# Optimization experiments

Hardware: AMD Instinct MI355X
Metric: run time of the kernel (lower is better)

## Reference

```python
import jax, jax.numpy as jnp
import numpy as np

B, N, F_DIM = 64, 4096, 64
K_SLOTS, D, N_ITERS = 8, 64, 3
EPS = 1e-8
LN_EPS = 1e-5  # torch LayerNorm default


def layernorm(x, g, b):
    mu = jnp.mean(x, axis=-1, keepdims=True)
    var = jnp.mean(jnp.square(x - mu), axis=-1, keepdims=True)
    return (x - mu) * jax.lax.rsqrt(var + LN_EPS) * g + b


def gru_cell(x, h, w_ih, w_hh, b_ih, b_hh):
    # torch.nn.GRUCell semantics; weights are [3D, D] with gate order r, z, n
    gi = x @ w_ih.T + b_ih
    gh = h @ w_hh.T + b_hh
    i_r, i_z, i_n = jnp.split(gi, 3, axis=-1)
    h_r, h_z, h_n = jnp.split(gh, 3, axis=-1)
    r = jax.nn.sigmoid(i_r + h_r)
    z = jax.nn.sigmoid(i_z + h_z)
    n = jnp.tanh(i_n + r * h_n)
    return (1.0 - z) * n + z * h


def setup_inputs() -> dict:
    key = jax.random.key(0)
    ks = jax.random.split(key, 16)
    f32 = jnp.float32
    s = 0.05  # small init scale for weights
    return {
        "inputs": jax.random.normal(ks[0], (B, N, F_DIM), f32),
        "slots_noise": jax.random.normal(ks[1], (B, K_SLOTS, D), f32),
        "slots_mu": jax.random.normal(ks[2], (1, 1, D), f32) * s,
        "slots_log_sigma": jax.random.normal(ks[3], (1, 1, D), f32) * s,
        "Wq": jax.random.normal(ks[4], (D, D), f32) * s,
        "Wk": jax.random.normal(ks[5], (D, F_DIM), f32) * s,
        "Wv": jax.random.normal(ks[6], (D, F_DIM), f32) * s,
        "gru_w_ih": jax.random.normal(ks[7], (3 * D, D), f32) * s,
        "gru_w_hh": jax.random.normal(ks[8], (3 * D, D), f32) * s,
        "gru_b_ih": jnp.zeros((3 * D,), f32),
        "gru_b_hh": jnp.zeros((3 * D,), f32),
        "mlp_w1": jax.random.normal(ks[9], (2 * D, D), f32) * s,
        "mlp_b1": jnp.zeros((2 * D,), f32),
        "mlp_w2": jax.random.normal(ks[10], (D, 2 * D), f32) * s,
        "mlp_b2": jnp.zeros((D,), f32),
        "ln_in_g": jnp.ones((F_DIM,), f32), "ln_in_b": jnp.zeros((F_DIM,), f32),
        "ln_slots_g": jnp.ones((D,), f32), "ln_slots_b": jnp.zeros((D,), f32),
        "ln_mlp_g": jnp.ones((D,), f32), "ln_mlp_b": jnp.zeros((D,), f32),
    }


def reference(inputs, slots_noise, slots_mu, slots_log_sigma, Wq, Wk, Wv,
              gru_w_ih, gru_w_hh, gru_b_ih, gru_b_hh,
              mlp_w1, mlp_b1, mlp_w2, mlp_b2,
              ln_in_g, ln_in_b, ln_slots_g, ln_slots_b, ln_mlp_g, ln_mlp_b):
    x = layernorm(inputs, ln_in_g, ln_in_b)          # [B, N, F]
    k = jnp.einsum('bnf,df->bnd', x, Wk)             # [B, N, D]
    v = jnp.einsum('bnf,df->bnd', x, Wv)             # [B, N, D]

    slots = slots_mu + jnp.exp(slots_log_sigma) * slots_noise  # [B, K, D]
    scale = D ** -0.5

    for _ in range(N_ITERS):
        slots_prev = slots
        s_n = layernorm(slots, ln_slots_g, ln_slots_b)
        q = jnp.einsum('bkd,ed->bke', s_n, Wq)                  # [B, K, D]
        attn_logits = jnp.einsum('bnd,bkd->bnk', k, q) * scale  # [B, N, K]
        attn = jax.nn.softmax(attn_logits, axis=-1) + EPS       # softmax over slots
        attn = attn / jnp.sum(attn, axis=1, keepdims=True)      # renormalize over N
        updates = jnp.einsum('bnk,bnd->bkd', attn, v)           # [B, K, D]
        slots = gru_cell(updates.reshape(-1, D), slots_prev.reshape(-1, D),
                         gru_w_ih, gru_w_hh, gru_b_ih, gru_b_hh).reshape(B, K_SLOTS, D)
        h = layernorm(slots, ln_mlp_g, ln_mlp_b)
        h = jax.nn.relu(h @ mlp_w1.T + mlp_b1) @ mlp_w2.T + mlp_b2
        slots = slots + h
    return slots
```

## Files before the change

### kernel.cpp

```cpp
#include <hip/hip_runtime.h>
#include <math.h>

#define NN 4096
#define LN_EPS 1e-5f
#define EPS 1e-8f

typedef unsigned short ushortT;
typedef unsigned int uintT;
typedef __attribute__((ext_vector_type(8))) short short8;
typedef __attribute__((ext_vector_type(4))) float f32x4;
typedef __attribute__((ext_vector_type(4))) unsigned short us4;

#define OFF_XN    0L
#define OFF_QU    8388608L
#define OFF_ACC   8421376L
#define OFF_COL   8519680L
#define OFF_SLOTS 8521216L
#define OFF_WIHT  8553984L
#define OFF_WHHT  8566272L
#define OFF_W1T   8578560L
#define OFF_W2T   8586752L
#define OFF_WQT   8594944L
#define OFF_WVT   8599040L
#define OFF_CNT   8603136L
#define OFF_RDY   8603328L

__device__ __forceinline__ float wredsum(float v) {
#pragma unroll
  for (int off = 32; off > 0; off >>= 1) v += __shfl_xor(v, off);
  return v;
}

__device__ __forceinline__ ushortT f2bf(float f) {
  uintT b = __float_as_uint(f);
  b += 0x7fff + ((b >> 16) & 1);
  return (ushortT)(b >> 16);
}

__device__ __forceinline__ uintT pack2bf(float lo, float hi) {
  return (uintT)f2bf(lo) | ((uintT)f2bf(hi) << 16);
}

__global__ __launch_bounds__(256) void k_prep(
    const float* __restrict__ w_ih, const float* __restrict__ w_hh,
    const float* __restrict__ w1, const float* __restrict__ w2,
    const float* __restrict__ Wq, const float* __restrict__ Wv,
    float* __restrict__ wihT, float* __restrict__ whhT,
    float* __restrict__ w1T, float* __restrict__ w2T, float* __restrict__ wqT,
    float* __restrict__ wvT, uintT* __restrict__ cnt, uintT* __restrict__ ready)
{
  int idx = blockIdx.x * 256 + threadIdx.x;
  if (idx < 12288) {
    int j = idx >> 6, f = idx & 63;
    wihT[f * 192 + j] = w_ih[idx];
  } else if (idx < 24576) {
    int i = idx - 12288; int j = i >> 6, f = i & 63;
    whhT[f * 192 + j] = w_hh[i];
  } else if (idx < 32768) {
    int i = idx - 24576; int j = i >> 6, f = i & 63;
    w1T[f * 128 + j] = w1[i];
  } else if (idx < 40960) {
    int i = idx - 32768; int d = i >> 7, j = i & 127;
    w2T[j * 64 + d] = w2[i];
  } else if (idx < 45056) {
    int i = idx - 40960; int e = i >> 6, d = i & 63;
    wqT[d * 64 + e] = Wq[i];
  } else if (idx < 49152) {
    int i = idx - 45056; int d = i >> 6, f = i & 63;
    wvT[f * 64 + d] = Wv[i];
  } else if (idx < 49344) {
    cnt[idx - 49152] = 0u;
  } else if (idx < 49408) {
    ready[idx - 49344] = 0u;
  }
}

__global__ __launch_bounds__(256) void k_ln_init(
    const float* __restrict__ inp,
    const float* __restrict__ g, const float* __restrict__ bbv,
    ushortT* __restrict__ xnG,
    const float* __restrict__ noise, const float* __restrict__ smu,
    const float* __restrict__ slsig, const float* __restrict__ wqT,
    const float* __restrict__ Wk,
    const float* __restrict__ g_sl, const float* __restrict__ b_sl,
    float* __restrict__ slots, uintT* __restrict__ qU,
    float* __restrict__ acc, float* __restrict__ colsum)
{
  __shared__ __align__(16) ushortT xnF[4096];
  const int tid = threadIdx.x;
  const int lane = tid & 63;
  const int wave = tid >> 6;

  if (blockIdx.x >= 4096) {
    const int bi = blockIdx.x - 4096;
    const int row = bi * 4 + wave;
    const int b = row >> 3, ks = row & 7;
    float* SI = (float*)&xnF[0];
    float* Sw = SI + (wave << 9);

    float s0 = fmaf(expf(slsig[lane]), noise[row * 64 + lane], smu[lane]);
    slots[row * 64 + lane] = s0;
#pragma unroll
    for (int it = 0; it < 3; ++it) {
      acc[it * 32768 + row * 64 + lane] = 0.f;
      if (lane == 0) colsum[it * 512 + row] = 0.f;
    }

    float mu = wredsum(s0) * (1.f / 64.f);
    float dx = s0 - mu;
    float var = wredsum(dx * dx) * (1.f / 64.f);
    float sn = dx * rsqrtf(var + LN_EPS) * g_sl[lane] + b_sl[lane];
    Sw[lane] = sn;
    float qe = 0.f;
#pragma unroll 16
    for (int d = 0; d < 64; ++d) qe = fmaf(Sw[d], wqT[d * 64 + lane], qe);
    Sw[64 + lane] = qe;
    float qp = 0.f;
#pragma unroll 16
    for (int e = 0; e < 64; ++e) qp = fmaf(Sw[64 + e], Wk[e * 64 + lane], qp);
    Sw[128 + lane] = qp * 0.125f;
    if (lane < 32) {
      const int kb = lane >> 4, lrow = (lane >> 2) & 3, j2 = lane & 3;
      const int fA = kb * 32 + lrow * 8 + 2 * j2;
      uintT u = pack2bf(Sw[128 + fA], Sw[128 + fA + 1]);
      qU[((b * 2 + kb) * 64 + lrow * 16 + ks) * 4 + j2] = u;
      qU[((b * 2 + kb) * 64 + lrow * 16 + 8 + ks) * 4 + j2] = 0u;
    }
    return;
  }

  const int l15 = lane & 15, q = lane >> 4;
  const int tile = blockIdx.x;
  const int b = tile >> 6;
  const int c = tile & 63;
  const int n0 = c << 6;
  const float* rowbase = inp + (((long)b * NN + n0) << 6);
  const float4 g4 = *(const float4*)&g[l15 << 2];
  const float4 b4 = *(const float4*)&bbv[l15 << 2];

#pragma unroll
  for (int i = 0; i < 4; ++i) {
    const int row = (wave << 4) + (i << 2) + q;
    float4 x = *(const float4*)&rowbase[(row << 6) + (l15 << 2)];
    float s = x.x + x.y + x.z + x.w;
    s += __shfl_xor(s, 1); s += __shfl_xor(s, 2);
    s += __shfl_xor(s, 4); s += __shfl_xor(s, 8);
    const float mu = s * (1.f / 64.f);
    float4 dx = {x.x - mu, x.y - mu, x.z - mu, x.w - mu};
    float ss = dx.x * dx.x + dx.y * dx.y + dx.z * dx.z + dx.w * dx.w;
    ss += __shfl_xor(ss, 1); ss += __shfl_xor(ss, 2);
    ss += __shfl_xor(ss, 4); ss += __shfl_xor(ss, 8);
    const float rs = rsqrtf(ss * (1.f / 64.f) + LN_EPS);
    us4 p = {f2bf(dx.x * rs * g4.x + b4.x), f2bf(dx.y * rs * g4.y + b4.y),
             f2bf(dx.z * rs * g4.z + b4.z), f2bf(dx.w * rs * g4.w + b4.w)};
    *(us4*)&xnF[((((wave << 1) + (l15 >> 3)) << 6) + (((l15 & 7) >> 1) << 4)
                 + (row & 15)) * 8 + ((l15 & 1) << 2)] = p;
  }
  __syncthreads();

  ushortT* dst = xnG + ((long)(b * 64 + c) << 12);
  short8 v0 = *(const short8*)&xnF[tid << 4];
  short8 v1 = *(const short8*)&xnF[(tid << 4) + 8];
  *(short8*)&dst[tid << 4] = v0;
  *(short8*)&dst[(tid << 4) + 8] = v1;
}

__global__ __launch_bounds__(256, 2) void k_attn(
    const ushortT* __restrict__ xnG, uintT* __restrict__ qU,
    float* __restrict__ acc, float* __restrict__ colsum,
    uintT* __restrict__ cnt, uintT* __restrict__ ready,
    float* __restrict__ slots,
    const float* __restrict__ wihT, const float* __restrict__ whhT,
    const float* __restrict__ w1T, const float* __restrict__ w2T,
    const float* __restrict__ wqT, const float* __restrict__ Wk,
    const float* __restrict__ wvT,
    const float* __restrict__ b_ih, const float* __restrict__ b_hh,
    const float* __restrict__ mb1, const float* __restrict__ mb2,
    const float* __restrict__ g_ml, const float* __restrict__ b_ml,
    const float* __restrict__ g_sl, const float* __restrict__ b_sl,
    float* __restrict__ dout)
{
  __shared__ __align__(16) ushortT XW[4][4096];
  __shared__ int lastFlag;
  const int tid = threadIdx.x;
  const int lane = tid & 63;
  const int wave = tid >> 6;
  const int l15 = lane & 15, q = lane >> 4;
  const int b = blockIdx.x >> 3;
  const int e = blockIdx.x & 7;

  ushortT* xT = &XW[wave][0];

  const ushortT* pc0 = xnG + ((long)(b * 64 + (e << 3) + wave) << 12);
  const ushortT* pc1 = pc0 + (4L << 12);

  short8 kA0[4][2], kA1[4][2];
#pragma unroll
  for (int mt = 0; mt < 4; ++mt)
#pragma unroll
    for (int kb = 0; kb < 2; ++kb) {
      kA0[mt][kb] = *(const short8*)&pc0[((mt * 2 + kb) * 64 + lane) << 3];
      kA1[mt][kb] = *(const short8*)&pc1[((mt * 2 + kb) * 64 + lane) << 3];
    }

  for (int it = 0; it < 3; ++it) {
    if (it > 0) {
      if (tid == 0) {
        while (atomicAdd(&ready[b], 0u) < (uintT)it) __builtin_amdgcn_s_sleep(2);
      }
      __syncthreads();
    }

    short8 qB[2];
#pragma unroll
    for (int kb = 0; kb < 2; ++kb) {
      uintT uu[4];
#pragma unroll
      for (int j2 = 0; j2 < 4; ++j2)
        uu[j2] = atomicAdd(&qU[((b * 2 + kb) * 64 + lane) * 4 + j2], 0u);
      qB[kb] = *(short8*)uu;
    }

    f32x4 accP[4];
#pragma unroll
    for (int nt = 0; nt < 4; ++nt) accP[nt] = (f32x4){0.f, 0.f, 0.f, 0.f};
    float csum = 0.f;

#pragma unroll
    for (int ch = 0; ch < 2; ++ch) {
      f32x4 accL[4];
#pragma unroll
      for (int mt = 0; mt < 4; ++mt) {
        const short8 a0 = ch ? kA1[mt][0] : kA0[mt][0];
        const short8 a1 = ch ? kA1[mt][1] : kA0[mt][1];
        accL[mt] = (f32x4){0.f, 0.f, 0.f, 0.f};
        accL[mt] = __builtin_amdgcn_mfma_f32_16x16x32_bf16(a0, qB[0], accL[mt], 0, 0, 0);
        accL[mt] = __builtin_amdgcn_mfma_f32_16x16x32_bf16(a1, qB[1], accL[mt], 0, 0, 0);
      }

      {
        const int h = ((lane >> 5) << 2) | (((lane & 15) >> 3) << 1) | ((lane >> 4) & 1);
        const int jp = lane & 7;
        const int lpA = (((lane >> 4) & 1) << 3) + (((lane & 15) >> 3) << 4);
#pragma unroll
        for (int mt = 0; mt < 4; ++mt)
#pragma unroll
          for (int kb = 0; kb < 2; ++kb) {
            const int fb = (kb * 4 + ((lane >> 5) << 1) + (mt >> 1)) << 9;
            const int lm = lpA + ((mt & 1) << 5);
            const short8 src8 = ch ? kA1[mt][kb] : kA0[mt][kb];
            const ushortT* src = (const ushortT*)&src8;
#pragma unroll
            for (int j = 0; j < 8; ++j)
              xT[fb + (((lm + j) ^ h) << 3) + jp] = src[j];
          }
      }
      short8 vB[4][2];
#pragma unroll
      for (int nt = 0; nt < 4; ++nt)
#pragma unroll
        for (int ks = 0; ks < 2; ++ks) {
          const int frag = nt * 2 + ks;
          const int hr = ((nt & 1) << 2) | (((lane >> 4) & 1) << 1) | ((lane >> 3) & 1);
          vB[nt][ks] = *(const short8*)&xT[(frag << 9) + ((lane ^ hr) << 3)];
        }

      ushortT* attnF = &XW[wave][0];
#pragma unroll
      for (int mt = 0; mt < 4; ++mt) {
        float av[4];
#pragma unroll
        for (int r = 0; r < 4; ++r) {
          float lv = accL[mt][r];
          float mx = lv;
          mx = fmaxf(mx, __shfl_xor(mx, 1));
          mx = fmaxf(mx, __shfl_xor(mx, 2));
          mx = fmaxf(mx, __shfl_xor(mx, 4));
          float ev = __expf(lv - mx);
          float sv = ev;
          sv += __shfl_xor(sv, 1); sv += __shfl_xor(sv, 2); sv += __shfl_xor(sv, 4);
          float a = ev * (1.f / sv) + EPS;
          av[r] = a;
          csum += a;
        }
        us4 p = {f2bf(av[0]), f2bf(av[1]), f2bf(av[2]), f2bf(av[3])};
        *(us4*)&attnF[((((mt >> 1) << 6) + (((mt & 1) * 2 + (q >> 1)) << 4)
                        + l15) << 3) + ((q & 1) << 2)] = p;
      }

      short8 pA0 = *(const short8*)&attnF[(0 * 64 + lane) << 3];
      short8 pA1 = *(const short8*)&attnF[(1 * 64 + lane) << 3];

#pragma unroll
      for (int nt = 0; nt < 4; ++nt) {
        accP[nt] = __builtin_amdgcn_mfma_f32_16x16x32_bf16(pA0, vB[nt][0], accP[nt], 0, 0, 0);
        accP[nt] = __builtin_amdgcn_mfma_f32_16x16x32_bf16(pA1, vB[nt][1], accP[nt], 0, 0, 0);
      }
    }

    csum += __shfl_xor(csum, 16);
    csum += __shfl_xor(csum, 32);

    float* accLw = (float*)&XW[wave][1024];
    float* colLw = (float*)&XW[wave][2048];
    if (q < 2) {
#pragma unroll
      for (int nt = 0; nt < 4; ++nt)
#pragma unroll
        for (int r = 0; r < 4; ++r)
          accLw[(q * 4 + r) * 64 + nt * 16 + l15] = accP[nt][r];
    }
    if (q == 0 && l15 < 8) colLw[l15] = csum;
    __syncthreads();

    float* accIt = acc + it * 32768;
    float* colIt = colsum + it * 512;
#pragma unroll
    for (int r = 0; r < 2; ++r) {
      const int o = tid + r * 256;
      const int kk = o >> 6, d = o & 63;
      float s = *((float*)&XW[0][1024] + kk * 64 + d)
              + *((float*)&XW[1][1024] + kk * 64 + d)
              + *((float*)&XW[2][1024] + kk * 64 + d)
              + *((float*)&XW[3][1024] + kk * 64 + d);
      atomicAdd(&accIt[(b * 8 + kk) * 64 + d], s);
    }
    if (tid < 8) {
      float s = *((float*)&XW[0][2048] + tid) + *((float*)&XW[1][2048] + tid)
              + *((float*)&XW[2][2048] + tid) + *((float*)&XW[3][2048] + tid);
      atomicAdd(&colIt[b * 8 + tid], s);
    }

    __syncthreads();
    if (tid == 0) lastFlag = (atomicAdd(&cnt[it * 64 + b], 1u) == 7u);
    __syncthreads();

    if (lastFlag) {
      const int ks0 = wave, ks1 = wave + 4;
      const int row0 = b * 8 + ks0, row1 = b * 8 + ks1;

      float csv0 = 0.f, csv1 = 0.f;
      if (lane == 0) {
        csv0 = atomicAdd(&colIt[row0], 0.f);
        csv1 = atomicAdd(&colIt[row1], 0.f);
      }
      csv0 = __shfl(csv0, 0); csv1 = __shfl(csv1, 0);
      const float t0 = atomicAdd(&accIt[row0 * 64 + lane], 0.f) / csv0;
      const float t1 = atomicAdd(&accIt[row1 * 64 + lane], 0.f) / csv1;
      const float h0 = atomicAdd(&slots[row0 * 64 + lane], 0.f);
      const float h1 = atomicAdd(&slots[row1 * 64 + lane], 0.f);

      float* S = (float*)&XW[wave][0];

      S[256 + lane] = t0; S[320 + lane] = t1;
      float u0 = 0.f, u1 = 0.f;
#pragma unroll 4
      for (int f = 0; f < 64; ++f) {
        const float wv = wvT[f * 64 + lane];
        u0 = fmaf(S[256 + f], wv, u0);
        u1 = fmaf(S[320 + f], wv, u1);
      }

      S[lane] = u0; S[64 + lane] = u1; S[128 + lane] = h0; S[192 + lane] = h1;

      float gir0 = b_ih[lane], giz0 = b_ih[64 + lane], gin0 = b_ih[128 + lane];
      float ghr0 = b_hh[lane], ghz0 = b_hh[64 + lane], ghn0 = b_hh[128 + lane];
      float gir1 = gir0, giz1 = giz0, gin1 = gin0;
      float ghr1 = ghr0, ghz1 = ghz0, ghn1 = ghn0;
#pragma unroll 4
      for (int f = 0; f < 64; ++f) {
        const float wr = wihT[f * 192 + lane], wz = wihT[f * 192 + 64 + lane],
                    wn = wihT[f * 192 + 128 + lane];
        const float vr = whhT[f * 192 + lane], vz = whhT[f * 192 + 64 + lane],
                    vn = whhT[f * 192 + 128 + lane];
        const float a0 = S[f], a1 = S[64 + f], c0 = S[128 + f], c1 = S[192 + f];
        gir0 = fmaf(a0, wr, gir0); gir1 = fmaf(a1, wr, gir1);
        giz0 = fmaf(a0, wz, giz0); giz1 = fmaf(a1, wz, giz1);
        gin0 = fmaf(a0, wn, gin0); gin1 = fmaf(a1, wn, gin1);
        ghr0 = fmaf(c0, vr, ghr0); ghr1 = fmaf(c1, vr, ghr1);
        ghz0 = fmaf(c0, vz, ghz0); ghz1 = fmaf(c1, vz, ghz1);
        ghn0 = fmaf(c0, vn, ghn0); ghn1 = fmaf(c1, vn, ghn1);
      }
      const float r0 = 1.f / (1.f + expf(-(gir0 + ghr0)));
      const float z0 = 1.f / (1.f + expf(-(giz0 + ghz0)));
      const float n0 = tanhf(fmaf(r0, ghn0, gin0));
      const float hn0 = (1.f - z0) * n0 + z0 * h0;
      const float r1 = 1.f / (1.f + expf(-(gir1 + ghr1)));
      const float z1 = 1.f / (1.f + expf(-(giz1 + ghz1)));
      const float n1 = tanhf(fmaf(r1, ghn1, gin1));
      const float hn1 = (1.f - z1) * n1 + z1 * h1;

      float mu0 = wredsum(hn0) * (1.f / 64.f);
      float dx0 = hn0 - mu0;
      float va0 = wredsum(dx0 * dx0) * (1.f / 64.f);
      const float ln0 = dx0 * rsqrtf(va0 + LN_EPS) * g_ml[lane] + b_ml[lane];
      float mu1 = wredsum(hn1) * (1.f / 64.f);
      float dx1 = hn1 - mu1;
      float va1 = wredsum(dx1 * dx1) * (1.f / 64.f);
      const float ln1 = dx1 * rsqrtf(va1 + LN_EPS) * g_ml[lane] + b_ml[lane];
      S[256 + lane] = ln0; S[320 + lane] = ln1;

      float h1a0 = mb1[lane], h1b0 = mb1[64 + lane];
      float h1a1 = h1a0, h1b1 = h1b0;
#pragma unroll 4
      for (int f = 0; f < 64; ++f) {
        const float wa = w1T[f * 128 + lane], wb = w1T[f * 128 + 64 + lane];
        const float l0 = S[256 + f], l1 = S[320 + f];
        h1a0 = fmaf(l0, wa, h1a0); h1a1 = fmaf(l1, wa, h1a1);
        h1b0 = fmaf(l0, wb, h1b0); h1b1 = fmaf(l1, wb, h1b1);
      }
      h1a0 = fmaxf(h1a0, 0.f); h1b0 = fmaxf(h1b0, 0.f);
      h1a1 = fmaxf(h1a1, 0.f); h1b1 = fmaxf(h1b1, 0.f);
      S[lane] = h1a0; S[64 + lane] = h1b0;
      S[128 + lane] = h1a1; S[192 + lane] = h1b1;

      float o0 = mb2[lane], o1 = mb2[lane];
#pragma unroll 4
      for (int j = 0; j < 128; ++j) {
        const float w2v = w2T[j * 64 + lane];
        o0 = fmaf(S[j], w2v, o0);
        o1 = fmaf(S[128 + j], w2v, o1);
      }
      const float sn0 = hn0 + o0;
      const float sn1 = hn1 + o1;

      if (it == 2) {
        dout[row0 * 64 + lane] = sn0;
        dout[row1 * 64 + lane] = sn1;
      } else {
        atomicExch(&slots[row0 * 64 + lane], sn0);
        atomicExch(&slots[row1 * 64 + lane], sn1);

        float m20 = wredsum(sn0) * (1.f / 64.f);
        float d20 = sn0 - m20;
        float v20 = wredsum(d20 * d20) * (1.f / 64.f);
        const float sq0 = d20 * rsqrtf(v20 + LN_EPS) * g_sl[lane] + b_sl[lane];
        float m21 = wredsum(sn1) * (1.f / 64.f);
        float d21 = sn1 - m21;
        float v21 = wredsum(d21 * d21) * (1.f / 64.f);
        const float sq1 = d21 * rsqrtf(v21 + LN_EPS) * g_sl[lane] + b_sl[lane];
        S[256 + lane] = sq0; S[320 + lane] = sq1;
        float qe0 = 0.f, qe1 = 0.f;
#pragma unroll 8
        for (int d = 0; d < 64; ++d) {
          const float wq = wqT[d * 64 + lane];
          qe0 = fmaf(S[256 + d], wq, qe0);
          qe1 = fmaf(S[320 + d], wq, qe1);
        }
        S[256 + lane] = qe0; S[320 + lane] = qe1;
        float qp0 = 0.f, qp1 = 0.f;
#pragma unroll 8
        for (int e2 = 0; e2 < 64; ++e2) {
          const float wk = Wk[e2 * 64 + lane];
          qp0 = fmaf(S[256 + e2], wk, qp0);
          qp1 = fmaf(S[320 + e2], wk, qp1);
        }
        S[384 + lane] = qp0 * 0.125f;
        S[448 + lane] = qp1 * 0.125f;
        {
          const int rr = lane >> 5, L5 = lane & 31;
          const int kb = L5 >> 4, lrow = (L5 >> 2) & 3, j2 = L5 & 3;
          const int fA = kb * 32 + lrow * 8 + 2 * j2;
          const int ksr = rr ? ks1 : ks0;
          uintT u = pack2bf(S[384 + rr * 64 + fA], S[384 + rr * 64 + fA + 1]);
          atomicExch(&qU[((b * 2 + kb) * 64 + lrow * 16 + ksr) * 4 + j2], u);
        }
        __syncthreads();
        if (tid == 0) atomicAdd(&ready[b], 1u);
      }
    }
  }
}

extern "C" void kernel_launch(void* const* d_in, const int* in_sizes, int n_in,
                              void* d_out, int out_size, void* d_ws, size_t ws_size,
                              hipStream_t stream) {
  const float* inp   = (const float*)d_in[0];
  const float* noise = (const float*)d_in[1];
  const float* smu   = (const float*)d_in[2];
  const float* slsig = (const float*)d_in[3];
  const float* Wq    = (const float*)d_in[4];
  const float* Wk    = (const float*)d_in[5];
  const float* Wv    = (const float*)d_in[6];
  const float* w_ih  = (const float*)d_in[7];
  const float* w_hh  = (const float*)d_in[8];
  const float* b_ih  = (const float*)d_in[9];
  const float* b_hh  = (const float*)d_in[10];
  const float* w1    = (const float*)d_in[11];
  const float* b1    = (const float*)d_in[12];
  const float* w2    = (const float*)d_in[13];
  const float* b2    = (const float*)d_in[14];
  const float* g_in  = (const float*)d_in[15];
  const float* bi_in = (const float*)d_in[16];
  const float* g_sl  = (const float*)d_in[17];
  const float* bi_sl = (const float*)d_in[18];
  const float* g_ml  = (const float*)d_in[19];
  const float* bi_ml = (const float*)d_in[20];

  float* ws      = (float*)d_ws;
  ushortT* xnG   = (ushortT*)(ws + OFF_XN);
  uintT* qU      = (uintT*)(ws + OFF_QU);
  float* ac      = ws + OFF_ACC;
  float* cs      = ws + OFF_COL;
  float* sl      = ws + OFF_SLOTS;
  float* wihT    = ws + OFF_WIHT;
  float* whhT    = ws + OFF_WHHT;
  float* w1T     = ws + OFF_W1T;
  float* w2T     = ws + OFF_W2T;
  float* wqT     = ws + OFF_WQT;
  float* wvT     = ws + OFF_WVT;
  uintT* cnt     = (uintT*)(ws + OFF_CNT);
  uintT* rdy     = (uintT*)(ws + OFF_RDY);

  k_prep<<<194, 256, 0, stream>>>(w_ih, w_hh, w1, w2, Wq, Wv,
                                  wihT, whhT, w1T, w2T, wqT, wvT, cnt, rdy);
  k_ln_init<<<4224, 256, 0, stream>>>(inp, g_in, bi_in, xnG,
                                      noise, smu, slsig, wqT, Wk, g_sl, bi_sl,
                                      sl, qU, ac, cs);
  k_attn<<<512, 256, 0, stream>>>(xnG, qU, ac, cs, cnt, rdy, sl,
                                  wihT, whhT, w1T, w2T, wqT, Wk, wvT,
                                  b_ih, b_hh, b1, b2, g_ml, bi_ml, g_sl, bi_sl,
                                  (float*)d_out);
}
```

Baseline: 259.7 us.

## Replace float atomics with per-block partial buffers and hoist V transpose

Each block now writes its partial attention-weighted sums and column sums to its own slot with coherent stores, instead of atomically adding into shared accumulators. The last-arriving block reduces the eight partials itself. q and slots are multi-buffered per iteration, so reads become plain vector loads rather than atomic reads. The LDS transpose of the V operand is hoisted out of the iteration loop into registers (vB0/vB1), which raises register pressure under the two-blocks-per-CU launch bound. It also drops the zeroing of accumulators in init and relies on hand-written cache-bypass asm for correctness.

```diff
diff --git a/kernel.cpp b/kernel.cpp
--- a/kernel.cpp
+++ b/kernel.cpp
@@ -9,21 +9,22 @@
 typedef unsigned int uintT;
 typedef __attribute__((ext_vector_type(8))) short short8;
 typedef __attribute__((ext_vector_type(4))) float f32x4;
+typedef __attribute__((ext_vector_type(2))) float f32x2;
 typedef __attribute__((ext_vector_type(4))) unsigned short us4;
 
 #define OFF_XN    0L
 #define OFF_QU    8388608L
-#define OFF_ACC   8421376L
-#define OFF_COL   8519680L
-#define OFF_SLOTS 8521216L
-#define OFF_WIHT  8553984L
-#define OFF_WHHT  8566272L
-#define OFF_W1T   8578560L
-#define OFF_W2T   8586752L
-#define OFF_WQT   8594944L
-#define OFF_WVT   8599040L
-#define OFF_CNT   8603136L
-#define OFF_RDY   8603328L
+#define OFF_AP    8486912L
+#define OFF_CP    9273344L
+#define OFF_SLOTS 9285632L
+#define OFF_WIHT  9383936L
+#define OFF_WHHT  9396224L
+#define OFF_W1T   9408512L
+#define OFF_W2T   9416704L
+#define OFF_WQT   9424896L
+#define OFF_WVT   9428992L
+#define OFF_CNT   9433088L
+#define OFF_RDY   9433280L
 
 __device__ __forceinline__ float wredsum(float v) {
 #pragma unroll
@@ -39,6 +40,25 @@
 
 __device__ __forceinline__ uintT pack2bf(float lo, float hi) {
   return (uintT)f2bf(lo) | ((uintT)f2bf(hi) << 16);
+}
+
+__device__ __forceinline__ void store2_coh(float* p, f32x2 v) {
+  asm volatile("global_store_dwordx2 %0, %1, off sc0 sc1" :: "v"(p), "v"(v) : "memory");
+}
+__device__ __forceinline__ void store1f_coh(float* p, float v) {
+  asm volatile("global_store_dword %0, %1, off sc0 sc1" :: "v"(p), "v"(v) : "memory");
+}
+__device__ __forceinline__ void store1u_coh(uintT* p, uintT v) {
+  asm volatile("global_store_dword %0, %1, off sc0 sc1" :: "v"(p), "v"(v) : "memory");
+}
+__device__ __forceinline__ uintT load1u_coh(const uintT* p) {
+  uintT r;
+  asm volatile("global_load_dword %0, %1, off sc0 sc1\n\t"
+               "s_waitcnt vmcnt(0)" : "=v"(r) : "v"(p) : "memory");
+  return r;
+}
+__device__ __forceinline__ void drain_vm() {
+  asm volatile("s_waitcnt vmcnt(0)" ::: "memory");
 }
 
 __global__ __launch_bounds__(256) void k_prep(
@@ -83,8 +103,7 @@
     const float* __restrict__ slsig, const float* __restrict__ wqT,
     const float* __restrict__ Wk,
     const float* __restrict__ g_sl, const float* __restrict__ b_sl,
-    float* __restrict__ slots, uintT* __restrict__ qU,
-    float* __restrict__ acc, float* __restrict__ colsum)
+    float* __restrict__ slotsV, uintT* __restrict__ qU)
 {
   __shared__ __align__(16) ushortT xnF[4096];
   const int tid = threadIdx.x;
@@ -99,12 +118,7 @@
     float* Sw = SI + (wave << 9);
 
     float s0 = fmaf(expf(slsig[lane]), noise[row * 64 + lane], smu[lane]);
-    slots[row * 64 + lane] = s0;
-#pragma unroll
-    for (int it = 0; it < 3; ++it) {
-      acc[it * 32768 + row * 64 + lane] = 0.f;
-      if (lane == 0) colsum[it * 512 + row] = 0.f;
-    }
+    slotsV[row * 64 + lane] = s0;
 
     float mu = wredsum(s0) * (1.f / 64.f);
     float dx = s0 - mu;
@@ -124,7 +138,9 @@
       const int fA = kb * 32 + lrow * 8 + 2 * j2;
       uintT u = pack2bf(Sw[128 + fA], Sw[128 + fA + 1]);
       qU[((b * 2 + kb) * 64 + lrow * 16 + ks) * 4 + j2] = u;
-      qU[((b * 2 + kb) * 64 + lrow * 16 + 8 + ks) * 4 + j2] = 0u;
+#pragma unroll
+      for (int v = 0; v < 3; ++v)
+        qU[v * 32768 + ((b * 2 + kb) * 64 + lrow * 16 + 8 + ks) * 4 + j2] = 0u;
     }
     return;
   }
@@ -167,9 +183,9 @@
 
 __global__ __launch_bounds__(256, 2) void k_attn(
     const ushortT* __restrict__ xnG, uintT* __restrict__ qU,
-    float* __restrict__ acc, float* __restrict__ colsum,
+    float* __restrict__ accPart, float* __restrict__ colPart,
     uintT* __restrict__ cnt, uintT* __restrict__ ready,
-    float* __restrict__ slots,
+    float* __restrict__ slotsV,
     const float* __restrict__ wihT, const float* __restrict__ whhT,
     const float* __restrict__ w1T, const float* __restrict__ w2T,
     const float* __restrict__ wqT, const float* __restrict__ Wk,
@@ -203,23 +219,50 @@
       kA1[mt][kb] = *(const short8*)&pc1[((mt * 2 + kb) * 64 + lane) << 3];
     }
 
+  short8 vB0[4][2], vB1[4][2];
+  {
+    const int h = ((lane >> 5) << 2) | (((lane & 15) >> 3) << 1) | ((lane >> 4) & 1);
+    const int jp = lane & 7;
+    const int lpA = (((lane >> 4) & 1) << 3) + (((lane & 15) >> 3) << 4);
+#pragma unroll
+    for (int ch = 0; ch < 2; ++ch) {
+#pragma unroll
+      for (int mt = 0; mt < 4; ++mt)
+#pragma unroll
+        for (int kb = 0; kb < 2; ++kb) {
+          const int fb = (kb * 4 + ((lane >> 5) << 1) + (mt >> 1)) << 9;
+          const int lm = lpA + ((mt & 1) << 5);
+          const short8 src8 = ch ? kA1[mt][kb] : kA0[mt][kb];
+          const ushortT* src = (const ushortT*)&src8;
+#pragma unroll
+          for (int j = 0; j < 8; ++j)
+            xT[fb + (((lm + j) ^ h) << 3) + jp] = src[j];
+        }
+#pragma unroll
+      for (int nt = 0; nt < 4; ++nt)
+#pragma unroll
+        for (int ks = 0; ks < 2; ++ks) {
+          const int frag = nt * 2 + ks;
+          const int hr = ((nt & 1) << 2) | (((lane >> 4) & 1) << 1) | ((lane >> 3) & 1);
+          short8 v = *(const short8*)&xT[(frag << 9) + ((lane ^ hr) << 3)];
+          if (ch) vB1[nt][ks] = v; else vB0[nt][ks] = v;
+        }
+    }
+  }
+
   for (int it = 0; it < 3; ++it) {
     if (it > 0) {
       if (tid == 0) {
-        while (atomicAdd(&ready[b], 0u) < (uintT)it) __builtin_amdgcn_s_sleep(2);
+        while (load1u_coh(&ready[b]) < (uintT)it) __builtin_amdgcn_s_sleep(2);
       }
       __syncthreads();
     }
 
+    const uintT* qIt = qU + it * 32768;
     short8 qB[2];
 #pragma unroll
-    for (int kb = 0; kb < 2; ++kb) {
-      uintT uu[4];
-#pragma unroll
-      for (int j2 = 0; j2 < 4; ++j2)
-        uu[j2] = atomicAdd(&qU[((b * 2 + kb) * 64 + lane) * 4 + j2], 0u);
-      qB[kb] = *(short8*)uu;
-    }
+    for (int kb = 0; kb < 2; ++kb)
+      qB[kb] = *(const short8*)&qIt[((b * 2 + kb) * 64 + lane) * 4];
 
     f32x4 accP[4];
 #pragma unroll
@@ -237,33 +280,6 @@
         accL[mt] = __builtin_amdgcn_mfma_f32_16x16x32_bf16(a0, qB[0], accL[mt], 0, 0, 0);
         accL[mt] = __builtin_amdgcn_mfma_f32_16x16x32_bf16(a1, qB[1], accL[mt], 0, 0, 0);
       }
-
-      {
-        const int h = ((lane >> 5) << 2) | (((lane & 15) >> 3) << 1) | ((lane >> 4) & 1);
-        const int jp = lane & 7;
-        const int lpA = (((lane >> 4) & 1) << 3) + (((lane & 15) >> 3) << 4);
-#pragma unroll
-        for (int mt = 0; mt < 4; ++mt)
-#pragma unroll
-          for (int kb = 0; kb < 2; ++kb) {
-            const int fb = (kb * 4 + ((lane >> 5) << 1) + (mt >> 1)) << 9;
-            const int lm = lpA + ((mt & 1) << 5);
-            const short8 src8 = ch ? kA1[mt][kb] : kA0[mt][kb];
-            const ushortT* src = (const ushortT*)&src8;
-#pragma unroll
-            for (int j = 0; j < 8; ++j)
-              xT[fb + (((lm + j) ^ h) << 3) + jp] = src[j];
-          }
-      }
-      short8 vB[4][2];
-#pragma unroll
-      for (int nt = 0; nt < 4; ++nt)
-#pragma unroll
-        for (int ks = 0; ks < 2; ++ks) {
-          const int frag = nt * 2 + ks;
-          const int hr = ((nt & 1) << 2) | (((lane >> 4) & 1) << 1) | ((lane >> 3) & 1);
-          vB[nt][ks] = *(const short8*)&xT[(frag << 9) + ((lane ^ hr) << 3)];
-        }
 
       ushortT* attnF = &XW[wave][0];
 #pragma unroll
@@ -293,8 +309,10 @@
 
 #pragma unroll
       for (int nt = 0; nt < 4; ++nt) {
-        accP[nt] = __builtin_amdgcn_mfma_f32_16x16x32_bf16(pA0, vB[nt][0], accP[nt], 0, 0, 0);
-        accP[nt] = __builtin_amdgcn_mfma_f32_16x16x32_bf16(pA1, vB[nt][1], accP[nt], 0, 0, 0);
+        const short8 v0 = ch ? vB1[nt][0] : vB0[nt][0];
+        const short8 v1 = ch ? vB1[nt][1] : vB0[nt][1];
+        accP[nt] = __builtin_amdgcn_mfma_f32_16x16x32_bf16(pA0, v0, accP[nt], 0, 0, 0);
+        accP[nt] = __builtin_amdgcn_mfma_f32_16x16x32_bf16(pA1, v1, accP[nt], 0, 0, 0);
       }
     }
 
@@ -313,24 +331,26 @@
     if (q == 0 && l15 < 8) colLw[l15] = csum;
     __syncthreads();
 
-    float* accIt = acc + it * 32768;
-    float* colIt = colsum + it * 512;
-#pragma unroll
-    for (int r = 0; r < 2; ++r) {
-      const int o = tid + r * 256;
-      const int kk = o >> 6, d = o & 63;
-      float s = *((float*)&XW[0][1024] + kk * 64 + d)
-              + *((float*)&XW[1][1024] + kk * 64 + d)
-              + *((float*)&XW[2][1024] + kk * 64 + d)
-              + *((float*)&XW[3][1024] + kk * 64 + d);
-      atomicAdd(&accIt[(b * 8 + kk) * 64 + d], s);
+    float* apIt = accPart + ((long)(it * 64 + b) * 8 + e) * 512;
+    float* cpIt = colPart + ((long)(it * 64 + b) * 8 + e) * 8;
+    {
+      const int o = tid * 2;
+      f32x2 s;
+#pragma unroll
+      for (int r = 0; r < 2; ++r) {
+        const int oo = o + r;
+        s[r] = *((float*)&XW[0][1024] + oo) + *((float*)&XW[1][1024] + oo)
+             + *((float*)&XW[2][1024] + oo) + *((float*)&XW[3][1024] + oo);
+      }
+      store2_coh(&apIt[o], s);
     }
     if (tid < 8) {
       float s = *((float*)&XW[0][2048] + tid) + *((float*)&XW[1][2048] + tid)
               + *((float*)&XW[2][2048] + tid) + *((float*)&XW[3][2048] + tid);
-      atomicAdd(&colIt[b * 8 + tid], s);
-    }
-
+      store1f_coh(&cpIt[tid], s);
+    }
+
+    drain_vm();
     __syncthreads();
     if (tid == 0) lastFlag = (atomicAdd(&cnt[it * 64 + b], 1u) == 7u);
     __syncthreads();
@@ -338,17 +358,21 @@
     if (lastFlag) {
       const int ks0 = wave, ks1 = wave + 4;
       const int row0 = b * 8 + ks0, row1 = b * 8 + ks1;
-
-      float csv0 = 0.f, csv1 = 0.f;
-      if (lane == 0) {
-        csv0 = atomicAdd(&colIt[row0], 0.f);
-        csv1 = atomicAdd(&colIt[row1], 0.f);
-      }
-      csv0 = __shfl(csv0, 0); csv1 = __shfl(csv1, 0);
-      const float t0 = atomicAdd(&accIt[row0 * 64 + lane], 0.f) / csv0;
-      const float t1 = atomicAdd(&accIt[row1 * 64 + lane], 0.f) / csv1;
-      const float h0 = atomicAdd(&slots[row0 * 64 + lane], 0.f);
-      const float h1 = atomicAdd(&slots[row1 * 64 + lane], 0.f);
+      const float* apB = accPart + (long)(it * 64 + b) * 8 * 512;
+      const float* cpB = colPart + (long)(it * 64 + b) * 8 * 8;
+      const float* slIt = slotsV + it * 32768;
+
+      float csv0 = 0.f, csv1 = 0.f, t0 = 0.f, t1 = 0.f;
+#pragma unroll
+      for (int ee = 0; ee < 8; ++ee) {
+        csv0 += cpB[ee * 8 + ks0];
+        csv1 += cpB[ee * 8 + ks1];
+        t0 += apB[ee * 512 + ks0 * 64 + lane];
+        t1 += apB[ee * 512 + ks1 * 64 + lane];
+      }
+      t0 /= csv0; t1 /= csv1;
+      const float h0 = slIt[row0 * 64 + lane];
+      const float h1 = slIt[row1 * 64 + lane];
 
       float* S = (float*)&XW[wave][0];
 
@@ -428,8 +452,9 @@
         dout[row0 * 64 + lane] = sn0;
         dout[row1 * 64 + lane] = sn1;
       } else {
-        atomicExch(&slots[row0 * 64 + lane], sn0);
-        atomicExch(&slots[row1 * 64 + lane], sn1);
+        float* slN = slotsV + (it + 1) * 32768;
+        store1f_coh(&slN[row0 * 64 + lane], sn0);
+        store1f_coh(&slN[row1 * 64 + lane], sn1);
 
         float m20 = wredsum(sn0) * (1.f / 64.f);
         float d20 = sn0 - m20;
@@ -458,13 +483,15 @@
         S[384 + lane] = qp0 * 0.125f;
         S[448 + lane] = qp1 * 0.125f;
         {
+          uintT* qN = qU + (it + 1) * 32768;
           const int rr = lane >> 5, L5 = lane & 31;
           const int kb = L5 >> 4, lrow = (L5 >> 2) & 3, j2 = L5 & 3;
           const int fA = kb * 32 + lrow * 8 + 2 * j2;
           const int ksr = rr ? ks1 : ks0;
           uintT u = pack2bf(S[384 + rr * 64 + fA], S[384 + rr * 64 + fA + 1]);
-          atomicExch(&qU[((b * 2 + kb) * 64 + lrow * 16 + ksr) * 4 + j2], u);
+          store1u_coh(&qN[((b * 2 + kb) * 64 + lrow * 16 + ksr) * 4 + j2], u);
         }
+        drain_vm();
         __syncthreads();
         if (tid == 0) atomicAdd(&ready[b], 1u);
       }
@@ -500,8 +527,8 @@
   float* ws      = (float*)d_ws;
   ushortT* xnG   = (ushortT*)(ws + OFF_XN);
   uintT* qU      = (uintT*)(ws + OFF_QU);
-  float* ac      = ws + OFF_ACC;
-  float* cs      = ws + OFF_COL;
+  float* ap      = ws + OFF_AP;
+  float* cp      = ws + OFF_CP;
   float* sl      = ws + OFF_SLOTS;
   float* wihT    = ws + OFF_WIHT;
   float* whhT    = ws + OFF_WHHT;
@@ -516,8 +543,8 @@
                                   wihT, whhT, w1T, w2T, wqT, wvT, cnt, rdy);
   k_ln_init<<<4224, 256, 0, stream>>>(inp, g_in, bi_in, xnG,
                                       noise, smu, slsig, wqT, Wk, g_sl, bi_sl,
-                                      sl, qU, ac, cs);
-  k_attn<<<512, 256, 0, stream>>>(xnG, qU, ac, cs, cnt, rdy, sl,
+                                      sl, qU);
+  k_attn<<<512, 256, 0, stream>>>(xnG, qU, ap, cp, cnt, rdy, sl,
                                   wihT, whhT, w1T, w2T, wqT, Wk, wvT,
                                   b_ih, b_hh, b1, b2, g_ml, bi_ml, g_sl, bi_sl,
                                   (float*)d_out);
```

Result: slower. 268.4 us (+3.3%).
